# Kernel optimization log

Measured on AMD Instinct MI355X. Metric: run time of the kernel, lower is better.

## Reference

```python
import jax, jax.numpy as jnp
import numpy as np

N = 10000       # nodes
E = 320000      # edges (before self-loops)
IN = 16         # in_channels


def _p(key, shape, scale=0.1):
    return jax.random.normal(key, shape, jnp.float32) * scale


def setup_inputs() -> dict:
    key = jax.random.key(0)
    ks = jax.random.split(key, 26)
    d = {}
    d["x"] = jax.random.normal(ks[0], (N, IN), jnp.float32)
    d["edge_index"] = jax.random.randint(ks[1], (2, E), 0, N, jnp.int32)
    d["JetRawPt"] = jax.random.normal(ks[2], (N, 1), jnp.float32)
    # conv1: GATConv(16 -> 32, heads=8)
    d["W1"] = _p(ks[3], (IN, 8 * 32)); d["a1s"] = _p(ks[4], (8, 32)); d["a1d"] = _p(ks[5], (8, 32)); d["b1"] = jnp.zeros((256,), jnp.float32)
    # conv2: GATConv(256 -> 32, heads=8)
    d["W2"] = _p(ks[6], (256, 8 * 32)); d["a2s"] = _p(ks[7], (8, 32)); d["a2d"] = _p(ks[8], (8, 32)); d["b2"] = jnp.zeros((256,), jnp.float32)
    # conv3: GATConv(256 -> 64, heads=12)
    d["W3"] = _p(ks[9], (256, 12 * 64)); d["a3s"] = _p(ks[10], (12, 64)); d["a3d"] = _p(ks[11], (12, 64)); d["b3"] = jnp.zeros((768,), jnp.float32)
    # linear_final: 256+256+768=1280 -> 1
    d["Wf"] = _p(ks[12], (1280, 1)); d["bf"] = jnp.zeros((1,), jnp.float32)
    # MLP: (16+1)->128->64->1
    d["M1w"] = _p(ks[13], (IN + 1, 128)); d["M1b"] = jnp.zeros((128,), jnp.float32)
    d["M2w"] = _p(ks[14], (128, 64)); d["M2b"] = jnp.zeros((64,), jnp.float32)
    d["M3w"] = _p(ks[15], (64, 1)); d["M3b"] = jnp.zeros((1,), jnp.float32)
    return d


def gat_layer(x, src, dst, W, a_s, a_d, b, H, C):
    # PyG GATConv (eval mode, self-loops already appended to src/dst)
    h = (x @ W).reshape(-1, H, C)                      # [N, H, C]
    al = jnp.sum(h * a_s, axis=-1)                     # [N, H] src-side score
    ar = jnp.sum(h * a_d, axis=-1)                     # [N, H] dst-side score
    e = jax.nn.leaky_relu(al[src] + ar[dst], 0.2)      # [Etot, H]
    m = jax.ops.segment_max(e, dst, num_segments=N)    # segment softmax over incoming edges
    ex = jnp.exp(e - m[dst])
    s = jax.ops.segment_sum(ex, dst, num_segments=N)
    alpha = ex / s[dst]                                # [Etot, H]
    out = jax.ops.segment_sum(h[src] * alpha[:, :, None], dst, num_segments=N)  # [N, H, C]
    return out.reshape(-1, H * C) + b


def reference(x, edge_index, JetRawPt, W1, a1s, a1d, b1, W2, a2s, a2d, b2,
              W3, a3s, a3d, b3, Wf, bf, M1w, M1b, M2w, M2b, M3w, M3b):
    loops = jnp.arange(N, dtype=edge_index.dtype)
    src = jnp.concatenate([edge_index[0], loops])
    dst = jnp.concatenate([edge_index[1], loops])
    x1 = jax.nn.relu(gat_layer(x, src, dst, W1, a1s, a1d, b1, 8, 32))
    x2 = jax.nn.relu(gat_layer(x1, src, dst, W2, a2s, a2d, b2, 8, 32))
    x3 = jax.nn.relu(gat_layer(x2, src, dst, W3, a3s, a3d, b3, 12, 64))
    xc = jnp.concatenate([x1, x2, x3], axis=1)         # [N, 1280]
    out1 = jax.nn.sigmoid(xc @ Wf + bf)                # [N, 1]
    xm = jnp.concatenate([x, out1], axis=1)            # [N, 17]
    h = jax.nn.relu(xm @ M1w + M1b)
    h = jax.nn.relu(h @ M2w + M2b)
    out2 = jax.nn.sigmoid(h @ M3w + M3b)               # [N, 1]
    return (out1, out2)
```

## Files before the change

kernel.cpp:

```cpp
#include <hip/hip_runtime.h>
#include <math.h>


typedef unsigned short bf16_t;
typedef __attribute__((ext_vector_type(8))) short bf16x8;
typedef __attribute__((ext_vector_type(4))) float f32x4;

__device__ inline float bf2f(bf16_t u) {
    union { unsigned int i; float f; } v; v.i = ((unsigned int)u) << 16; return v.f;
}
__device__ inline float u2f(unsigned int x) {
    union { unsigned int i; float f; } v; v.i = x; return v.f;
}
__device__ inline bf16_t f2bf(float f) {
    union { float f; unsigned int i; } v; v.f = f;
    unsigned int r = v.i + 0x7FFF + ((v.i >> 16) & 1);
    return (bf16_t)(r >> 16);
}


__global__ void zero_i32(int* p, int n) {
    int i = blockIdx.x * blockDim.x + threadIdx.x;
    if (i < n) p[i] = 0;
}

__global__ void count_edges(const int* __restrict__ ei, int E, int Nn,
                            int* __restrict__ counts) {
    int e = blockIdx.x * blockDim.x + threadIdx.x;
    if (e >= E + Nn) return;
    int dst = (e < E) ? ei[E + e] : (e - E);
    atomicAdd(&counts[dst], 1);
}

__global__ __launch_bounds__(1024) void scan_rowptr(const int* __restrict__ counts,
                                                    int* __restrict__ rowptr, int n) {
    const int IPT = (n + 1023) / 1024;
    int t = threadIdx.x;
    int base = t * IPT;
    int loc[16];
    int run = 0;
#pragma unroll
    for (int i = 0; i < 16; i++) {
        if (i >= IPT) break;
        int idx = base + i;
        int v = (idx < n) ? counts[idx] : 0;
        loc[i] = run;
        run += v;
    }
    int lane = t & 63, wid = t >> 6;
    int v = run;
    for (int off = 1; off < 64; off <<= 1) {
        int u = __shfl_up(v, off, 64);
        if (lane >= off) v += u;
    }
    __shared__ int wsum[16];
    __shared__ int woff[16];
    if (lane == 63) wsum[wid] = v;
    __syncthreads();
    if (t == 0) { int s = 0; for (int i = 0; i < 16; i++) { woff[i] = s; s += wsum[i]; } }
    __syncthreads();
    int excl = v - run + woff[wid];
#pragma unroll
    for (int i = 0; i < 16; i++) {
        if (i >= IPT) break;
        int idx = base + i;
        if (idx < n) rowptr[idx] = excl + loc[i];
    }
    if (t == 1023) rowptr[n] = excl + run;
}

__global__ void fill_edges(const int* __restrict__ ei, int E, int Nn,
                           const int* __restrict__ rowptr, int* __restrict__ cursor,
                           int* __restrict__ edge_src) {
    int e = blockIdx.x * blockDim.x + threadIdx.x;
    if (e >= E + Nn) return;
    int src, dst;
    if (e < E) { src = ei[e]; dst = ei[E + e]; }
    else       { src = e - E; dst = src; }
    int pos = atomicAdd(&cursor[dst], 1);
    edge_src[rowptr[dst] + pos] = src;
}

__global__ __launch_bounds__(256) void transpose_cast2(const float* __restrict__ W2,
                                                       bf16_t* __restrict__ Wt2,
                                                       const float* __restrict__ W3,
                                                       bf16_t* __restrict__ Wt3) {
    __shared__ float tile[16][17];
    const float* W; bf16_t* Wt; int Nc, n0;
    if (blockIdx.y < 16) { W = W2; Wt = Wt2; Nc = 256; n0 = blockIdx.y * 16; }
    else                 { W = W3; Wt = Wt3; Nc = 768; n0 = (blockIdx.y - 16) * 16; }
    int k0 = blockIdx.x * 16;
    int tx = threadIdx.x & 15, ty = threadIdx.x >> 4;
    tile[ty][tx] = W[(size_t)(k0 + ty) * Nc + n0 + tx];
    __syncthreads();
    Wt[(size_t)(n0 + ty) * 256 + k0 + tx] = f2bf(tile[tx][ty]);
}

__global__ __launch_bounds__(256) void gemm_f32_bf16(const float* __restrict__ A,
                                                     const float* __restrict__ B,
                                                     bf16_t* __restrict__ Cm,
                                                     int M, int K, int Nc) {
    __shared__ float As[16][64];
    __shared__ float Bs[16][64];
    int t  = threadIdx.x;
    int tx = t & 15, ty = t >> 4;
    int row0 = blockIdx.y * 64, col0 = blockIdx.x * 64;
    int a_r = t >> 2, a_c = (t & 3) * 4;
    int b_r = t >> 4, b_c = (t & 15) * 4;

    float acc[4][4];
#pragma unroll
    for (int i = 0; i < 4; i++)
#pragma unroll
        for (int j = 0; j < 4; j++) acc[i][j] = 0.f;

    for (int kt = 0; kt < K; kt += 16) {
        float4 av = make_float4(0.f, 0.f, 0.f, 0.f);
        int gr = row0 + a_r;
        if (gr < M) av = *(const float4*)(A + (size_t)gr * K + kt + a_c);
        As[a_c + 0][a_r] = av.x;
        As[a_c + 1][a_r] = av.y;
        As[a_c + 2][a_r] = av.z;
        As[a_c + 3][a_r] = av.w;
        float4 bv = *(const float4*)(B + (size_t)(kt + b_r) * Nc + col0 + b_c);
        *(float4*)&Bs[b_r][b_c] = bv;
        __syncthreads();
#pragma unroll
        for (int k = 0; k < 16; k++) {
            float4 a4 = *(const float4*)&As[k][ty * 4];
            float4 b4 = *(const float4*)&Bs[k][tx * 4];
            float aa[4] = {a4.x, a4.y, a4.z, a4.w};
            float bb[4] = {b4.x, b4.y, b4.z, b4.w};
#pragma unroll
            for (int i = 0; i < 4; i++)
#pragma unroll
                for (int j = 0; j < 4; j++) acc[i][j] += aa[i] * bb[j];
        }
        __syncthreads();
    }
#pragma unroll
    for (int i = 0; i < 4; i++) {
        int gr = row0 + ty * 4 + i;
        if (gr < M) {
            ushort4 v;
            v.x = f2bf(acc[i][0]); v.y = f2bf(acc[i][1]);
            v.z = f2bf(acc[i][2]); v.w = f2bf(acc[i][3]);
            *(ushort4*)(Cm + (size_t)gr * Nc + col0 + tx * 4) = v;
        }
    }
}

__global__ __launch_bounds__(256) void gemm_mfma(const bf16_t* __restrict__ A,
                                                 const bf16_t* __restrict__ Bt,
                                                 bf16_t* __restrict__ Cm,
                                                 int M, int K, int Nc) {
    int wave = threadIdx.x >> 6, lane = threadIdx.x & 63;
    int quad = lane >> 4, l16 = lane & 15;
    int m0 = blockIdx.y * 128 + wave * 32;
    int n0 = blockIdx.x * 64;

    f32x4 acc[2][4];
    f32x4 z = {0.f, 0.f, 0.f, 0.f};
#pragma unroll
    for (int i = 0; i < 2; i++)
#pragma unroll
        for (int j = 0; j < 4; j++) acc[i][j] = z;

    int r0 = m0 + l16;       if (r0 >= M) r0 = M - 1;
    int r1 = m0 + 16 + l16;  if (r1 >= M) r1 = M - 1;
    const bf16_t* Ap0 = A + (size_t)r0 * K + quad * 8;
    const bf16_t* Ap1 = A + (size_t)r1 * K + quad * 8;
    const bf16_t* Bp0 = Bt + (size_t)(n0 + 0  + l16) * K + quad * 8;
    const bf16_t* Bp1 = Bt + (size_t)(n0 + 16 + l16) * K + quad * 8;
    const bf16_t* Bp2 = Bt + (size_t)(n0 + 32 + l16) * K + quad * 8;
    const bf16_t* Bp3 = Bt + (size_t)(n0 + 48 + l16) * K + quad * 8;

    for (int kt = 0; kt < K; kt += 32) {
        bf16x8 a0 = *(const bf16x8*)(Ap0 + kt);
        bf16x8 a1 = *(const bf16x8*)(Ap1 + kt);
        bf16x8 b0 = *(const bf16x8*)(Bp0 + kt);
        bf16x8 b1 = *(const bf16x8*)(Bp1 + kt);
        bf16x8 b2 = *(const bf16x8*)(Bp2 + kt);
        bf16x8 b3 = *(const bf16x8*)(Bp3 + kt);
        acc[0][0] = __builtin_amdgcn_mfma_f32_16x16x32_bf16(a0, b0, acc[0][0], 0, 0, 0);
        acc[1][0] = __builtin_amdgcn_mfma_f32_16x16x32_bf16(a1, b0, acc[1][0], 0, 0, 0);
        acc[0][1] = __builtin_amdgcn_mfma_f32_16x16x32_bf16(a0, b1, acc[0][1], 0, 0, 0);
        acc[1][1] = __builtin_amdgcn_mfma_f32_16x16x32_bf16(a1, b1, acc[1][1], 0, 0, 0);
        acc[0][2] = __builtin_amdgcn_mfma_f32_16x16x32_bf16(a0, b2, acc[0][2], 0, 0, 0);
        acc[1][2] = __builtin_amdgcn_mfma_f32_16x16x32_bf16(a1, b2, acc[1][2], 0, 0, 0);
        acc[0][3] = __builtin_amdgcn_mfma_f32_16x16x32_bf16(a0, b3, acc[0][3], 0, 0, 0);
        acc[1][3] = __builtin_amdgcn_mfma_f32_16x16x32_bf16(a1, b3, acc[1][3], 0, 0, 0);
    }
#pragma unroll
    for (int i = 0; i < 2; i++)
#pragma unroll
        for (int j = 0; j < 4; j++)
#pragma unroll
            for (int r = 0; r < 4; r++) {
                int gr = m0 + i * 16 + quad * 4 + r;
                if (gr < M) Cm[(size_t)gr * Nc + n0 + j * 16 + l16] = f2bf(acc[i][j][r]);
            }
}

template <int H, int C>
__global__ void gat_scores(const bf16_t* __restrict__ hbuf, const float* __restrict__ a_s,
                           const float* __restrict__ a_d, float* __restrict__ al,
                           float* __restrict__ ar, int n) {
    int i = blockIdx.x * blockDim.x + threadIdx.x;
    if (i >= n * H) return;
    int node = i / H, h = i - node * H;
    const bf16_t* hr = hbuf + (size_t)node * (H * C) + h * C;
    const float* as_ = a_s + h * C;
    const float* ad_ = a_d + h * C;
    float sa = 0.f, sd = 0.f;
#pragma unroll
    for (int c = 0; c < C; c += 4) {
        ushort4 u = *(const ushort4*)(hr + c);
        float v0 = bf2f(u.x), v1 = bf2f(u.y), v2 = bf2f(u.z), v3 = bf2f(u.w);
        sa += v0 * as_[c] + v1 * as_[c + 1] + v2 * as_[c + 2] + v3 * as_[c + 3];
        sd += v0 * ad_[c] + v1 * ad_[c + 1] + v2 * ad_[c + 2] + v3 * ad_[c + 3];
    }
    al[i] = sa;
    ar[i] = sd;
}

template <int H>
__global__ __launch_bounds__(256) void alpha_node(const float* __restrict__ al,
                                                  const float* __restrict__ ar,
                                                  const int* __restrict__ rowptr,
                                                  const int* __restrict__ esrc,
                                                  float* __restrict__ alpha,
                                                  int n, int Etot) {
    int node = (blockIdx.x * blockDim.x + threadIdx.x) >> 6;
    if (node >= n) return;
    int lane = threadIdx.x & 63;

    float arv[H];
#pragma unroll
    for (int h4 = 0; h4 < H; h4 += 4) {
        float4 t = *(const float4*)(ar + (size_t)node * H + h4);
        arv[h4] = t.x; arv[h4 + 1] = t.y; arv[h4 + 2] = t.z; arv[h4 + 3] = t.w;
    }
    int beg = rowptr[node], end = rowptr[node + 1];
    float p0[H], p1[H], s[H];
#pragma unroll
    for (int h = 0; h < H; h++) { p0[h] = 0.f; p1[h] = 0.f; s[h] = 0.f; }

    int j0 = beg + lane;
    if (j0 < end) {
        const float* alr = al + (size_t)esrc[j0] * H;
#pragma unroll
        for (int h4 = 0; h4 < H; h4 += 4) {
            float4 t = *(const float4*)(alr + h4);
            float e;
            e = t.x + arv[h4];     e = fmaxf(e, 0.2f * e); p0[h4]     = __expf(fminf(e, 60.f));
            e = t.y + arv[h4 + 1]; e = fmaxf(e, 0.2f * e); p0[h4 + 1] = __expf(fminf(e, 60.f));
            e = t.z + arv[h4 + 2]; e = fmaxf(e, 0.2f * e); p0[h4 + 2] = __expf(fminf(e, 60.f));
            e = t.w + arv[h4 + 3]; e = fmaxf(e, 0.2f * e); p0[h4 + 3] = __expf(fminf(e, 60.f));
        }
#pragma unroll
        for (int h = 0; h < H; h++) s[h] += p0[h];
    }
    int j1 = j0 + 64;
    if (j1 < end) {
        const float* alr = al + (size_t)esrc[j1] * H;
#pragma unroll
        for (int h4 = 0; h4 < H; h4 += 4) {
            float4 t = *(const float4*)(alr + h4);
            float e;
            e = t.x + arv[h4];     e = fmaxf(e, 0.2f * e); p1[h4]     = __expf(fminf(e, 60.f));
            e = t.y + arv[h4 + 1]; e = fmaxf(e, 0.2f * e); p1[h4 + 1] = __expf(fminf(e, 60.f));
            e = t.z + arv[h4 + 2]; e = fmaxf(e, 0.2f * e); p1[h4 + 2] = __expf(fminf(e, 60.f));
            e = t.w + arv[h4 + 3]; e = fmaxf(e, 0.2f * e); p1[h4 + 3] = __expf(fminf(e, 60.f));
        }
#pragma unroll
        for (int h = 0; h < H; h++) s[h] += p1[h];
    }
    for (int j = j0 + 128; j < end; j += 64) {
        const float* alr = al + (size_t)esrc[j] * H;
#pragma unroll
        for (int h = 0; h < H; h++) {
            float e = alr[h] + arv[h];
            e = fmaxf(e, 0.2f * e);
            float p = __expf(fminf(e, 60.f));
            alpha[(size_t)h * Etot + j] = p;
            s[h] += p;
        }
    }
#pragma unroll
    for (int h = 0; h < H; h++) {
        float v = s[h];
#pragma unroll
        for (int off = 32; off > 0; off >>= 1) v += __shfl_xor(v, off, 64);
        s[h] = 1.f / v;
    }
    if (j0 < end) {
#pragma unroll
        for (int h = 0; h < H; h++) alpha[(size_t)h * Etot + j0] = p0[h] * s[h];
    }
    if (j1 < end) {
#pragma unroll
        for (int h = 0; h < H; h++) alpha[(size_t)h * Etot + j1] = p1[h] * s[h];
    }
    for (int j = j0 + 128; j < end; j += 64) {
#pragma unroll
        for (int h = 0; h < H; h++) alpha[(size_t)h * Etot + j] *= s[h];
    }
}

template <int HC_, int C>
__global__ __launch_bounds__(256) void gat_agg(
    const bf16_t* __restrict__ hbuf, const float* __restrict__ alpha,
    const int* __restrict__ rowptr, const int* __restrict__ esrc,
    const float* __restrict__ bias, bf16_t* __restrict__ outb,
    int n, int Etot, int nodeblocks) {
    int group = blockIdx.x / nodeblocks;
    int nb    = blockIdx.x - group * nodeblocks;
    int node  = nb * 4 + (threadIdx.x >> 6);
    if (node >= n) return;
    int lane = threadIdx.x & 63;
    int sub  = lane >> 4;
    int cl   = lane & 15;
    int gc   = group * 128 + cl * 8;
    int head = gc / C;
    const bf16_t* hb = hbuf + gc;
    const float*  ap = alpha + (size_t)head * Etot;

    float acc[8];
#pragma unroll
    for (int i = 0; i < 8; i++) acc[i] = 0.f;

    int beg = rowptr[node], end = rowptr[node + 1];
    int deg = end - beg;

    int e0 = 0, e1 = 0;
    {
        int i0 = beg + lane;
        if (i0 < end) e0 = esrc[i0];
        int i1 = beg + 64 + lane;
        if (i1 < end) e1 = esrc[i1];
    }
    int npre  = deg < 128 ? deg : 128;
    int nfull = npre >> 3;

    if (nfull > 0) {
        int esel0 = e0;
        int s0 = __shfl(esel0, sub, 64);
        int s1 = __shfl(esel0, sub + 4, 64);
        float a0 = ap[beg + sub], a1 = ap[beg + sub + 4];
        bf16x8 u0 = *(const bf16x8*)(hb + (size_t)s0 * HC_);
        bf16x8 u1 = *(const bf16x8*)(hb + (size_t)s1 * HC_);
        for (int it = 1; it < nfull; ++it) {
            int kb = it * 8;
            int esel = (kb < 64) ? e0 : e1;
            int t0 = __shfl(esel, (kb + sub) & 63, 64);
            int t1 = __shfl(esel, (kb + sub + 4) & 63, 64);
            float b0v = ap[beg + kb + sub], b1v = ap[beg + kb + sub + 4];
            bf16x8 v0 = *(const bf16x8*)(hb + (size_t)t0 * HC_);
            bf16x8 v1 = *(const bf16x8*)(hb + (size_t)t1 * HC_);
            const unsigned int* d0 = (const unsigned int*)&u0;
            const unsigned int* d1 = (const unsigned int*)&u1;
#pragma unroll
            for (int i = 0; i < 4; i++) {
                acc[2 * i]     += a0 * u2f(d0[i] << 16);
                acc[2 * i + 1] += a0 * u2f(d0[i] & 0xffff0000u);
                acc[2 * i]     += a1 * u2f(d1[i] << 16);
                acc[2 * i + 1] += a1 * u2f(d1[i] & 0xffff0000u);
            }
            u0 = v0; u1 = v1; a0 = b0v; a1 = b1v;
        }
        const unsigned int* d0 = (const unsigned int*)&u0;
        const unsigned int* d1 = (const unsigned int*)&u1;
#pragma unroll
        for (int i = 0; i < 4; i++) {
            acc[2 * i]     += a0 * u2f(d0[i] << 16);
            acc[2 * i + 1] += a0 * u2f(d0[i] & 0xffff0000u);
            acc[2 * i]     += a1 * u2f(d1[i] << 16);
            acc[2 * i + 1] += a1 * u2f(d1[i] & 0xffff0000u);
        }
    }
    for (int j = beg + (nfull << 3) + sub; j < end; j += 4) {
        int s0 = esrc[j];
        float a0 = ap[j];
        bf16x8 u0 = *(const bf16x8*)(hb + (size_t)s0 * HC_);
        const unsigned int* d0 = (const unsigned int*)&u0;
#pragma unroll
        for (int i = 0; i < 4; i++) {
            acc[2 * i]     += a0 * u2f(d0[i] << 16);
            acc[2 * i + 1] += a0 * u2f(d0[i] & 0xffff0000u);
        }
    }
#pragma unroll
    for (int i = 0; i < 8; i++) {
        acc[i] += __shfl_xor(acc[i], 16, 64);
        acc[i] += __shfl_xor(acc[i], 32, 64);
    }
    if (sub == 0) {
        float4 b0 = *(const float4*)(bias + gc);
        float4 b1 = *(const float4*)(bias + gc + 4);
        float bb[8] = {b0.x, b0.y, b0.z, b0.w, b1.x, b1.y, b1.z, b1.w};
        bf16x8 outv;
        unsigned short* ov = (unsigned short*)&outv;
#pragma unroll
        for (int i = 0; i < 8; i++) ov[i] = f2bf(fmaxf(acc[i] + bb[i], 0.f));
        *(bf16x8*)(outb + (size_t)node * HC_ + gc) = outv;
    }
}

__global__ __launch_bounds__(256) void head_fused(
    const float* __restrict__ x, const bf16_t* __restrict__ x1b,
    const bf16_t* __restrict__ x2b, const bf16_t* __restrict__ x3b,
    const float* __restrict__ Wf, const float* __restrict__ bfc,
    const float* __restrict__ M1w, const float* __restrict__ M1b,
    const float* __restrict__ M2w, const float* __restrict__ M2b,
    const float* __restrict__ M3w, const float* __restrict__ M3b,
    float* __restrict__ out1, float* __restrict__ out2, int n) {
    __shared__ float h1s[4][128];
    int w    = threadIdx.x >> 6;
    int lane = threadIdx.x & 63;
    int node = blockIdx.x * 4 + w;
    bool valid = node < n;
    int nd = valid ? node : 0;

    float s = 0.f;
    {
        ushort4 u = *(const ushort4*)(x1b + (size_t)nd * 256 + lane * 4);
        const float* wv = Wf + lane * 4;
        s += bf2f(u.x) * wv[0] + bf2f(u.y) * wv[1] + bf2f(u.z) * wv[2] + bf2f(u.w) * wv[3];
    }
    {
        ushort4 u = *(const ushort4*)(x2b + (size_t)nd * 256 + lane * 4);
        const float* wv = Wf + 256 + lane * 4;
        s += bf2f(u.x) * wv[0] + bf2f(u.y) * wv[1] + bf2f(u.z) * wv[2] + bf2f(u.w) * wv[3];
    }
#pragma unroll
    for (int i = 0; i < 3; i++) {
        int k = i * 256 + lane * 4;
        ushort4 u = *(const ushort4*)(x3b + (size_t)nd * 768 + k);
        const float* wv = Wf + 512 + k;
        s += bf2f(u.x) * wv[0] + bf2f(u.y) * wv[1] + bf2f(u.z) * wv[2] + bf2f(u.w) * wv[3];
    }
#pragma unroll
    for (int off = 32; off > 0; off >>= 1) s += __shfl_xor(s, off, 64);
    float so = 1.f / (1.f + __expf(-(s + bfc[0])));
    if (lane == 0 && valid) out1[node] = so;

    float xm[17];
#pragma unroll
    for (int k = 0; k < 16; k++) xm[k] = x[nd * 16 + k];
    xm[16] = so;

    float a0 = M1b[lane], a1 = M1b[lane + 64];
#pragma unroll
    for (int k = 0; k < 17; k++) {
        a0 += xm[k] * M1w[k * 128 + lane];
        a1 += xm[k] * M1w[k * 128 + lane + 64];
    }
    h1s[w][lane]      = fmaxf(a0, 0.f);
    h1s[w][lane + 64] = fmaxf(a1, 0.f);
    __syncthreads();

    float b0 = M2b[lane];
#pragma unroll 16
    for (int k = 0; k < 128; k++) b0 += h1s[w][k] * M2w[k * 64 + lane];
    b0 = fmaxf(b0, 0.f);

    float p = b0 * M3w[lane];
#pragma unroll
    for (int off = 32; off > 0; off >>= 1) p += __shfl_xor(p, off, 64);
    if (lane == 0 && valid) out2[node] = 1.f / (1.f + __expf(-(p + M3b[0])));
}

extern "C" void kernel_launch(void* const* d_in, const int* in_sizes, int n_in,
                              void* d_out, int out_size, void* d_ws, size_t ws_size,
                              hipStream_t stream) {
    const float* x   = (const float*)d_in[0];
    const int*   ei  = (const int*)d_in[1];
    const float* W1  = (const float*)d_in[3];
    const float* a1s = (const float*)d_in[4];
    const float* a1d = (const float*)d_in[5];
    const float* b1  = (const float*)d_in[6];
    const float* W2  = (const float*)d_in[7];
    const float* a2s = (const float*)d_in[8];
    const float* a2d = (const float*)d_in[9];
    const float* b2  = (const float*)d_in[10];
    const float* W3  = (const float*)d_in[11];
    const float* a3s = (const float*)d_in[12];
    const float* a3d = (const float*)d_in[13];
    const float* b3  = (const float*)d_in[14];
    const float* Wf  = (const float*)d_in[15];
    const float* bf  = (const float*)d_in[16];
    const float* M1w = (const float*)d_in[17];
    const float* M1b = (const float*)d_in[18];
    const float* M2w = (const float*)d_in[19];
    const float* M2b = (const float*)d_in[20];
    const float* M3w = (const float*)d_in[21];
    const float* M3b = (const float*)d_in[22];

    const int N = in_sizes[0] / 16;
    const int E = in_sizes[1] / 2;
    const int Etot = E + N;

    char* base = (char*)d_ws;
    size_t off = 0;
    auto carve = [&](size_t bytes) {
        char* p = base + off;
        off = (off + bytes + 255) & ~(size_t)255;
        return p;
    };
    bf16_t* hbuf   = (bf16_t*)carve((size_t)N * 768 * 2);
    bf16_t* x1b    = (bf16_t*)carve((size_t)N * 256 * 2);
    bf16_t* x2b    = (bf16_t*)carve((size_t)N * 256 * 2);
    bf16_t* x3b    = (bf16_t*)carve((size_t)N * 768 * 2);
    bf16_t* Wt2    = (bf16_t*)carve((size_t)256 * 256 * 2);
    bf16_t* Wt3    = (bf16_t*)carve((size_t)256 * 768 * 2);
    float*  al     = (float*)carve((size_t)N * 12 * 4);
    float*  ar     = (float*)carve((size_t)N * 12 * 4);
    float*  alphab = (float*)carve((size_t)Etot * 12 * 4);
    int*    rowptr = (int*)carve((size_t)(N + 1) * 4);
    int*    cnt2   = (int*)carve((size_t)(2 * N) * 4);
    int*    counts = cnt2;
    int*    cursor = cnt2 + N;
    int*    esrc   = (int*)carve((size_t)Etot * 4);
    (void)ws_size;

    float* out1 = (float*)d_out;
    float* out2 = (float*)d_out + N;

    const int TB = 256;
    int eb = (Etot + TB - 1) / TB;
    int nodeblocks = (N + 3) / 4;

    zero_i32<<<(2 * N + TB - 1) / TB, TB, 0, stream>>>(cnt2, 2 * N);
    count_edges<<<eb, TB, 0, stream>>>(ei, E, N, counts);
    scan_rowptr<<<1, 1024, 0, stream>>>(counts, rowptr, N);
    fill_edges<<<eb, TB, 0, stream>>>(ei, E, N, rowptr, cursor, esrc);
    transpose_cast2<<<dim3(16, 64), TB, 0, stream>>>(W2, Wt2, W3, Wt3);

    gemm_f32_bf16<<<dim3(4, (N + 63) / 64), TB, 0, stream>>>(x, W1, hbuf, N, 16, 256);
    gat_scores<8, 32><<<(N * 8 + TB - 1) / TB, TB, 0, stream>>>(hbuf, a1s, a1d, al, ar, N);
    alpha_node<8><<<nodeblocks, TB, 0, stream>>>(al, ar, rowptr, esrc, alphab, N, Etot);
    gat_agg<256, 32><<<2 * nodeblocks, TB, 0, stream>>>(hbuf, alphab, rowptr, esrc, b1, x1b, N, Etot, nodeblocks);

    gemm_mfma<<<dim3(4, (N + 127) / 128), TB, 0, stream>>>(x1b, Wt2, hbuf, N, 256, 256);
    gat_scores<8, 32><<<(N * 8 + TB - 1) / TB, TB, 0, stream>>>(hbuf, a2s, a2d, al, ar, N);
    alpha_node<8><<<nodeblocks, TB, 0, stream>>>(al, ar, rowptr, esrc, alphab, N, Etot);
    gat_agg<256, 32><<<2 * nodeblocks, TB, 0, stream>>>(hbuf, alphab, rowptr, esrc, b2, x2b, N, Etot, nodeblocks);

    gemm_mfma<<<dim3(12, (N + 127) / 128), TB, 0, stream>>>(x2b, Wt3, hbuf, N, 256, 768);
    gat_scores<12, 64><<<(N * 12 + TB - 1) / TB, TB, 0, stream>>>(hbuf, a3s, a3d, al, ar, N);
    alpha_node<12><<<nodeblocks, TB, 0, stream>>>(al, ar, rowptr, esrc, alphab, N, Etot);
    gat_agg<768, 64><<<6 * nodeblocks, TB, 0, stream>>>(hbuf, alphab, rowptr, esrc, b3, x3b, N, Etot, nodeblocks);

    head_fused<<<nodeblocks, TB, 0, stream>>>(x, x1b, x2b, x3b, Wf, bf,
                                              M1w, M1b, M2w, M2b, M3w, M3b, out1, out2, N);
}
```

Measured before the change: 348.0 us.

## Fuse attention score computation into GEMM epilogues and batch gather loads in aggregation

Removes the separate gat_scores kernels. Each GEMM (the fp32 first-layer one and the MFMA ones) now computes the per-head src and dst attention dot products from its fp32 accumulators in the epilogue, using lane shuffles to reduce across the head's columns. This saves three launches and the re-read of the bf16 hidden buffer, and the scores now come from fp32 values rather than rounded bf16. The aggregation kernel also issues eight independent gathers per 32-edge batch instead of a two-deep software pipeline, for more memory-level parallelism at the cost of extra registers.

```diff
diff --git a/kernel.cpp b/kernel.cpp
--- a/kernel.cpp
+++ b/kernel.cpp
@@ -96,10 +96,14 @@
     Wt[(size_t)(n0 + ty) * 256 + k0 + tx] = f2bf(tile[tx][ty]);
 }
 
-__global__ __launch_bounds__(256) void gemm_f32_bf16(const float* __restrict__ A,
-                                                     const float* __restrict__ B,
-                                                     bf16_t* __restrict__ Cm,
-                                                     int M, int K, int Nc) {
+__global__ __launch_bounds__(256) void gemm_f32_sc(const float* __restrict__ A,
+                                                   const float* __restrict__ B,
+                                                   bf16_t* __restrict__ Cm,
+                                                   const float* __restrict__ a_s,
+                                                   const float* __restrict__ a_d,
+                                                   float* __restrict__ al,
+                                                   float* __restrict__ ar,
+                                                   int M, int K, int Nc, int H) {
     __shared__ float As[16][64];
     __shared__ float Bs[16][64];
     int t  = threadIdx.x;
@@ -138,9 +142,23 @@
         }
         __syncthreads();
     }
+    float4 asv = *(const float4*)(a_s + col0 + tx * 4);
+    float4 adv = *(const float4*)(a_d + col0 + tx * 4);
 #pragma unroll
     for (int i = 0; i < 4; i++) {
         int gr = row0 + ty * 4 + i;
+        float sa = acc[i][0] * asv.x + acc[i][1] * asv.y + acc[i][2] * asv.z + acc[i][3] * asv.w;
+        float sd = acc[i][0] * adv.x + acc[i][1] * adv.y + acc[i][2] * adv.z + acc[i][3] * adv.w;
+#pragma unroll
+        for (int off = 4; off > 0; off >>= 1) {
+            sa += __shfl_xor(sa, off, 64);
+            sd += __shfl_xor(sd, off, 64);
+        }
+        if ((tx == 0 || tx == 8) && gr < M) {
+            int h = (col0 >> 5) + (tx >> 3);
+            al[gr * H + h] = sa;
+            ar[gr * H + h] = sd;
+        }
         if (gr < M) {
             ushort4 v;
             v.x = f2bf(acc[i][0]); v.y = f2bf(acc[i][1]);
@@ -150,10 +168,15 @@
     }
 }
 
-__global__ __launch_bounds__(256) void gemm_mfma(const bf16_t* __restrict__ A,
-                                                 const bf16_t* __restrict__ Bt,
-                                                 bf16_t* __restrict__ Cm,
-                                                 int M, int K, int Nc) {
+template <int C_>
+__global__ __launch_bounds__(256) void gemm_mfma_sc(const bf16_t* __restrict__ A,
+                                                    const bf16_t* __restrict__ Bt,
+                                                    bf16_t* __restrict__ Cm,
+                                                    const float* __restrict__ a_s,
+                                                    const float* __restrict__ a_d,
+                                                    float* __restrict__ al,
+                                                    float* __restrict__ ar,
+                                                    int M, int K, int Nc, int H) {
     int wave = threadIdx.x >> 6, lane = threadIdx.x & 63;
     int quad = lane >> 4, l16 = lane & 15;
     int m0 = blockIdx.y * 128 + wave * 32;
@@ -191,6 +214,54 @@
         acc[0][3] = __builtin_amdgcn_mfma_f32_16x16x32_bf16(a0, b3, acc[0][3], 0, 0, 0);
         acc[1][3] = __builtin_amdgcn_mfma_f32_16x16x32_bf16(a1, b3, acc[1][3], 0, 0, 0);
     }
+
+    float asv[4], adv[4];
+#pragma unroll
+    for (int j = 0; j < 4; j++) {
+        asv[j] = a_s[n0 + j * 16 + l16];
+        adv[j] = a_d[n0 + j * 16 + l16];
+    }
+#pragma unroll
+    for (int i = 0; i < 2; i++)
+#pragma unroll
+        for (int r = 0; r < 4; r++) {
+            int gr = m0 + i * 16 + quad * 4 + r;
+            if (C_ == 64) {
+                float sa = acc[i][0][r] * asv[0] + acc[i][1][r] * asv[1]
+                         + acc[i][2][r] * asv[2] + acc[i][3][r] * asv[3];
+                float sd = acc[i][0][r] * adv[0] + acc[i][1][r] * adv[1]
+                         + acc[i][2][r] * adv[2] + acc[i][3][r] * adv[3];
+#pragma unroll
+                for (int off = 8; off > 0; off >>= 1) {
+                    sa += __shfl_xor(sa, off, 64);
+                    sd += __shfl_xor(sd, off, 64);
+                }
+                if (l16 == 0 && gr < M) {
+                    int h = n0 >> 6;
+                    al[gr * H + h] = sa;
+                    ar[gr * H + h] = sd;
+                }
+            } else {
+                float saA = acc[i][0][r] * asv[0] + acc[i][1][r] * asv[1];
+                float saB = acc[i][2][r] * asv[2] + acc[i][3][r] * asv[3];
+                float sdA = acc[i][0][r] * adv[0] + acc[i][1][r] * adv[1];
+                float sdB = acc[i][2][r] * adv[2] + acc[i][3][r] * adv[3];
+#pragma unroll
+                for (int off = 8; off > 0; off >>= 1) {
+                    saA += __shfl_xor(saA, off, 64);
+                    saB += __shfl_xor(saB, off, 64);
+                    sdA += __shfl_xor(sdA, off, 64);
+                    sdB += __shfl_xor(sdB, off, 64);
+                }
+                if (l16 == 0 && gr < M) {
+                    int h = n0 >> 5;
+                    al[gr * H + h]     = saA;
+                    ar[gr * H + h]     = sdA;
+                    al[gr * H + h + 1] = saB;
+                    ar[gr * H + h + 1] = sdB;
+                }
+            }
+        }
 #pragma unroll
     for (int i = 0; i < 2; i++)
 #pragma unroll
@@ -200,28 +271,6 @@
                 int gr = m0 + i * 16 + quad * 4 + r;
                 if (gr < M) Cm[(size_t)gr * Nc + n0 + j * 16 + l16] = f2bf(acc[i][j][r]);
             }
-}
-
-template <int H, int C>
-__global__ void gat_scores(const bf16_t* __restrict__ hbuf, const float* __restrict__ a_s,
-                           const float* __restrict__ a_d, float* __restrict__ al,
-                           float* __restrict__ ar, int n) {
-    int i = blockIdx.x * blockDim.x + threadIdx.x;
-    if (i >= n * H) return;
-    int node = i / H, h = i - node * H;
-    const bf16_t* hr = hbuf + (size_t)node * (H * C) + h * C;
-    const float* as_ = a_s + h * C;
-    const float* ad_ = a_d + h * C;
-    float sa = 0.f, sd = 0.f;
-#pragma unroll
-    for (int c = 0; c < C; c += 4) {
-        ushort4 u = *(const ushort4*)(hr + c);
-        float v0 = bf2f(u.x), v1 = bf2f(u.y), v2 = bf2f(u.z), v3 = bf2f(u.w);
-        sa += v0 * as_[c] + v1 * as_[c + 1] + v2 * as_[c + 2] + v3 * as_[c + 3];
-        sd += v0 * ad_[c] + v1 * ad_[c + 1] + v2 * ad_[c + 2] + v3 * ad_[c + 3];
-    }
-    al[i] = sa;
-    ar[i] = sd;
 }
 
 template <int H>
@@ -340,35 +389,39 @@
         int i1 = beg + 64 + lane;
         if (i1 < end) e1 = esrc[i1];
     }
-    int npre  = deg < 128 ? deg : 128;
-    int nfull = npre >> 3;
-
-    if (nfull > 0) {
-        int esel0 = e0;
-        int s0 = __shfl(esel0, sub, 64);
-        int s1 = __shfl(esel0, sub + 4, 64);
-        float a0 = ap[beg + sub], a1 = ap[beg + sub + 4];
+    int npre = deg < 128 ? deg : 128;
+    int nb32 = npre >> 5;
+
+    for (int it = 0; it < nb32; ++it) {
+        int kb = it << 5;
+        int esel = (kb & 64) ? e1 : e0;
+        int sidx[8]; float av[8]; bf16x8 u[8];
+#pragma unroll
+        for (int q = 0; q < 8; q++) sidx[q] = __shfl(esel, (kb + sub + 4 * q) & 63, 64);
+#pragma unroll
+        for (int q = 0; q < 8; q++) av[q] = ap[beg + kb + sub + 4 * q];
+#pragma unroll
+        for (int q = 0; q < 8; q++) u[q] = *(const bf16x8*)(hb + (size_t)sidx[q] * HC_);
+#pragma unroll
+        for (int q = 0; q < 8; q++) {
+            const unsigned int* d = (const unsigned int*)&u[q];
+#pragma unroll
+            for (int i = 0; i < 4; i++) {
+                acc[2 * i]     += av[q] * u2f(d[i] << 16);
+                acc[2 * i + 1] += av[q] * u2f(d[i] & 0xffff0000u);
+            }
+        }
+    }
+    int done = nb32 << 5;
+    int np8 = (npre - done) >> 3;
+    for (int p = 0; p < np8; ++p) {
+        int kb = done + (p << 3);
+        int esel = (kb & 64) ? e1 : e0;
+        int s0 = __shfl(esel, (kb + sub) & 63, 64);
+        int s1 = __shfl(esel, (kb + sub + 4) & 63, 64);
+        float a0 = ap[beg + kb + sub], a1 = ap[beg + kb + sub + 4];
         bf16x8 u0 = *(const bf16x8*)(hb + (size_t)s0 * HC_);
         bf16x8 u1 = *(const bf16x8*)(hb + (size_t)s1 * HC_);
-        for (int it = 1; it < nfull; ++it) {
-            int kb = it * 8;
-            int esel = (kb < 64) ? e0 : e1;
-            int t0 = __shfl(esel, (kb + sub) & 63, 64);
-            int t1 = __shfl(esel, (kb + sub + 4) & 63, 64);
-            float b0v = ap[beg + kb + sub], b1v = ap[beg + kb + sub + 4];
-            bf16x8 v0 = *(const bf16x8*)(hb + (size_t)t0 * HC_);
-            bf16x8 v1 = *(const bf16x8*)(hb + (size_t)t1 * HC_);
-            const unsigned int* d0 = (const unsigned int*)&u0;
-            const unsigned int* d1 = (const unsigned int*)&u1;
-#pragma unroll
-            for (int i = 0; i < 4; i++) {
-                acc[2 * i]     += a0 * u2f(d0[i] << 16);
-                acc[2 * i + 1] += a0 * u2f(d0[i] & 0xffff0000u);
-                acc[2 * i]     += a1 * u2f(d1[i] << 16);
-                acc[2 * i + 1] += a1 * u2f(d1[i] & 0xffff0000u);
-            }
-            u0 = v0; u1 = v1; a0 = b0v; a1 = b1v;
-        }
         const unsigned int* d0 = (const unsigned int*)&u0;
         const unsigned int* d1 = (const unsigned int*)&u1;
 #pragma unroll
@@ -379,7 +432,8 @@
             acc[2 * i + 1] += a1 * u2f(d1[i] & 0xffff0000u);
         }
     }
-    for (int j = beg + (nfull << 3) + sub; j < end; j += 4) {
+    done += np8 << 3;
+    for (int j = beg + done + sub; j < end; j += 4) {
         int s0 = esrc[j];
         float a0 = ap[j];
         bf16x8 u0 = *(const bf16x8*)(hb + (size_t)s0 * HC_);
@@ -537,18 +591,15 @@
     fill_edges<<<eb, TB, 0, stream>>>(ei, E, N, rowptr, cursor, esrc);
     transpose_cast2<<<dim3(16, 64), TB, 0, stream>>>(W2, Wt2, W3, Wt3);
 
-    gemm_f32_bf16<<<dim3(4, (N + 63) / 64), TB, 0, stream>>>(x, W1, hbuf, N, 16, 256);
-    gat_scores<8, 32><<<(N * 8 + TB - 1) / TB, TB, 0, stream>>>(hbuf, a1s, a1d, al, ar, N);
+    gemm_f32_sc<<<dim3(4, (N + 63) / 64), TB, 0, stream>>>(x, W1, hbuf, a1s, a1d, al, ar, N, 16, 256, 8);
     alpha_node<8><<<nodeblocks, TB, 0, stream>>>(al, ar, rowptr, esrc, alphab, N, Etot);
     gat_agg<256, 32><<<2 * nodeblocks, TB, 0, stream>>>(hbuf, alphab, rowptr, esrc, b1, x1b, N, Etot, nodeblocks);
 
-    gemm_mfma<<<dim3(4, (N + 127) / 128), TB, 0, stream>>>(x1b, Wt2, hbuf, N, 256, 256);
-    gat_scores<8, 32><<<(N * 8 + TB - 1) / TB, TB, 0, stream>>>(hbuf, a2s, a2d, al, ar, N);
+    gemm_mfma_sc<32><<<dim3(4, (N + 127) / 128), TB, 0, stream>>>(x1b, Wt2, hbuf, a2s, a2d, al, ar, N, 256, 256, 8);
     alpha_node<8><<<nodeblocks, TB, 0, stream>>>(al, ar, rowptr, esrc, alphab, N, Etot);
     gat_agg<256, 32><<<2 * nodeblocks, TB, 0, stream>>>(hbuf, alphab, rowptr, esrc, b2, x2b, N, Etot, nodeblocks);
 
-    gemm_mfma<<<dim3(12, (N + 127) / 128), TB, 0, stream>>>(x2b, Wt3, hbuf, N, 256, 768);
-    gat_scores<12, 64><<<(N * 12 + TB - 1) / TB, TB, 0, stream>>>(hbuf, a3s, a3d, al, ar, N);
+    gemm_mfma_sc<64><<<dim3(12, (N + 127) / 128), TB, 0, stream>>>(x2b, Wt3, hbuf, a3s, a3d, al, ar, N, 256, 768, 12);
     alpha_node<12><<<nodeblocks, TB, 0, stream>>>(al, ar, rowptr, esrc, alphab, N, Etot);
     gat_agg<768, 64><<<6 * nodeblocks, TB, 0, stream>>>(hbuf, alphab, rowptr, esrc, b3, x3b, N, Etot, nodeblocks);
 
```

Measured after the change: 360.9 us. +3.7%, slower.
